# Kernel tuning notes

Measured on AMD Instinct MI355X. Metric: run time of the kernel, lower is better.

Reference implementation:

```python
import jax, jax.numpy as jnp
import numpy as np

# dims
N, D, H, C = 50000, 64, 4, 64          # nodes, node feat (=out_channels), heads, head dim
E, P, EPN, V, NA = 300000, 20000, 300000, 2000, 128  # node edges, paths, path->node edges, vehicles, n_actor
HC = H * C
HID = (NA + D) // 2                    # PathPredNet hidden (size // 2)


def _layernorm(x, g, b, eps=1e-5):
    m = x.mean(-1, keepdims=True)
    v = ((x - m) ** 2).mean(-1, keepdims=True)
    return (x - m) * jax.lax.rsqrt(v + eps) * g + b


def _segment_softmax(logits, seg, num):
    m = jax.ops.segment_max(logits, seg, num_segments=num)
    e = jnp.exp(logits - m[seg])
    s = jax.ops.segment_sum(e, seg, num_segments=num)
    return e / (s[seg] + 1e-16)


def setup_inputs() -> dict:
    key = jax.random.key(0)
    ks = jax.random.split(key, 32)

    def lin(k, i, o):
        s = 1.0 / np.sqrt(i)
        return jax.random.uniform(k, (i, o), minval=-s, maxval=s, dtype=jnp.float32)

    inp = {}
    inp['x'] = jax.random.normal(ks[0], (N, D), dtype=jnp.float32)
    inp['edge_index'] = jax.random.randint(ks[1], (2, E), 0, N)
    inp['path_node_u'] = jax.random.randint(ks[2], (EPN,), 0, P)
    inp['path_node_v'] = jax.random.randint(ks[3], (EPN,), 0, N)
    inp['veh_path_u'] = jax.random.randint(ks[4], (P,), 0, V)
    inp['actors'] = jax.random.normal(ks[5], (V, NA), dtype=jnp.float32)
    # TransformerConv params
    inp['Wq'] = lin(ks[6], D, HC);  inp['bq'] = jnp.zeros((HC,), jnp.float32)
    inp['Wk'] = lin(ks[7], D, HC);  inp['bk'] = jnp.zeros((HC,), jnp.float32)
    inp['Wv'] = lin(ks[8], D, HC);  inp['bv'] = jnp.zeros((HC,), jnp.float32)
    inp['Wskip'] = lin(ks[9], HC, D); inp['bskip'] = jnp.zeros((D,), jnp.float32)
    inp['ln1_g'] = jnp.ones((D,), jnp.float32); inp['ln1_b'] = jnp.zeros((D,), jnp.float32)
    inp['Wf1'] = lin(ks[10], D, 2 * D); inp['bf1'] = jnp.zeros((2 * D,), jnp.float32)
    inp['Wf2'] = lin(ks[11], 2 * D, D); inp['bf2'] = jnp.zeros((D,), jnp.float32)
    inp['ln2_g'] = jnp.ones((D,), jnp.float32); inp['ln2_b'] = jnp.zeros((D,), jnp.float32)
    # PathPredNet params (non-latent: size = n_actor + n_map)
    inp['Wp1'] = lin(ks[12], NA + D, HID); inp['bp1'] = jnp.zeros((HID,), jnp.float32)
    inp['gn_g'] = jnp.ones((HID,), jnp.float32); inp['gn_b'] = jnp.zeros((HID,), jnp.float32)
    inp['Wp2'] = lin(ks[13], HID, 1); inp['bp2'] = jnp.zeros((1,), jnp.float32)
    return inp


def reference(x, edge_index, path_node_u, path_node_v, veh_path_u, actors,
              Wq, bq, Wk, bk, Wv, bv, Wskip, bskip, ln1_g, ln1_b,
              Wf1, bf1, Wf2, bf2, ln2_g, ln2_b,
              Wp1, bp1, gn_g, gn_b, Wp2, bp2):
    # ---- TransformerConv (multi-head graph attention over edge list) ----
    q = (x @ Wq + bq).reshape(N, H, C)
    k = (x @ Wk + bk).reshape(N, H, C)
    v = (x @ Wv + bv).reshape(N, H, C)
    src, dst = edge_index[0], edge_index[1]
    alpha = (q[dst] * k[src]).sum(-1) / np.sqrt(C)           # [E, H]
    a = _segment_softmax(alpha, dst, N)                      # edge softmax per target node
    msg = v[src] * a[:, :, None]                             # [E, H, C]
    out = jax.ops.segment_sum(msg, dst, num_segments=N).reshape(N, HC)
    out = out @ Wskip + bskip                                # lin_skip (concat path)
    out = _layernorm(out + x, ln1_g, ln1_b)                  # norm1(out + x)
    ff = jax.nn.relu(out @ Wf1 + bf1) @ Wf2 + bf2            # feed_forward
    out2 = _layernorm(ff + x, ln2_g, ln2_b)                  # norm2(ff + x) -- residual is x as in source

    # ---- path features: aggregate member-node features per path (path->node edges) ----
    psum = jax.ops.segment_sum(out2[path_node_v], path_node_u, num_segments=P)
    cnt = jax.ops.segment_sum(jnp.ones((EPN,), out2.dtype), path_node_u, num_segments=P)
    paths = psum / jnp.maximum(cnt, 1.0)[:, None]            # [P, D]

    # ---- PathPredNet: logit per (veh, path) edge; veh_path_u[p] is owner vehicle ----
    feat = jnp.concatenate([paths, actors[veh_path_u]], axis=-1)  # [P, D + NA]
    h = feat @ Wp1 + bp1
    hm = h.mean(-1, keepdims=True)
    hv = ((h - hm) ** 2).mean(-1, keepdims=True)
    h = jax.nn.relu((h - hm) * jax.lax.rsqrt(hv + 1e-5) * gn_g + gn_b)   # GN with ng=1
    logits = (h @ Wp2 + bp2).squeeze(-1)                     # [P]

    # ---- scatter_softmax over each vehicle's candidate paths (ucb_sample_path) ----
    probs = _segment_softmax(logits, veh_path_u, V)          # [P]
    return (out2, probs)
```

## Files before the change

### kernel.cpp

```cpp
#include <hip/hip_runtime.h>
#include <hip/hip_bf16.h>
#include <math.h>

#define N_    50000
#define D_    64
#define H_    4
#define C_    64
#define HC_   256
#define E_    300000
#define P_    20000
#define EPN_  300000
#define V_    2000
#define NA_   128
#define HID_  96

#define CN_        70000
#define SCAN_CHUNK 4096
#define SCAN_NB    18

typedef __attribute__((ext_vector_type(8))) short bf16x8;
typedef __attribute__((ext_vector_type(4))) float f32x4;

__device__ __forceinline__ unsigned short f2bf(float f) {
    unsigned u = __float_as_uint(f);
    unsigned r = (u + 0x7fffu + ((u >> 16) & 1u)) >> 16;
    return (unsigned short)r;
}
__device__ __forceinline__ float bf2f(unsigned short u) {
    return __uint_as_float(((unsigned)u) << 16);
}

__device__ __forceinline__ void atomicMaxFloat(float* addr, float value) {
    if (value >= 0.f)
        atomicMax((int*)addr, __float_as_int(value));
    else
        atomicMin((unsigned int*)addr, __float_as_uint(value));
}

__device__ __forceinline__ float waveRedSum(float v) {
    #pragma unroll
    for (int off = 32; off; off >>= 1) v += __shfl_xor(v, off);
    return v;
}
__device__ __forceinline__ int waveRedSumI(int v) {
    #pragma unroll
    for (int off = 32; off; off >>= 1) v += __shfl_xor(v, off);
    return v;
}

__global__ void neginf_kernel(float* __restrict__ p, int n) {
    int i = blockIdx.x * 256 + threadIdx.x;
    if (i < n) p[i] = __int_as_float(0xFF800000);
}

__global__ void hist_kernel(const int* __restrict__ ei, const int* __restrict__ pnu,
                            int* __restrict__ deg_n, int* __restrict__ deg_p) {
    int i = blockIdx.x * 256 + threadIdx.x;
    if (i < E_) {
        atomicAdd(&deg_n[ei[E_ + i]], 1);
    } else if (i < E_ + EPN_) {
        atomicAdd(&deg_p[pnu[i - E_]], 1);
    }
}

__global__ __launch_bounds__(256) void scan_part_kernel(
    const int* __restrict__ cdeg, int* __restrict__ bsum) {
    __shared__ int wred[4];
    int b = blockIdx.x, t = threadIdx.x;
    int base = b * SCAN_CHUNK + t * 16;
    int s = 0;
    #pragma unroll
    for (int j = 0; j < 16; j += 4) {
        int idx = base + j;
        if (idx + 3 < CN_) {
            int4 vv = *(const int4*)(cdeg + idx);
            s += vv.x + vv.y + vv.z + vv.w;
        } else {
            #pragma unroll
            for (int q = 0; q < 4; ++q) if (idx + q < CN_) s += cdeg[idx + q];
        }
    }
    s = waveRedSumI(s);
    if ((t & 63) == 0) wred[t >> 6] = s;
    __syncthreads();
    if (t == 0) bsum[b] = wred[0] + wred[1] + wred[2] + wred[3];
}

__global__ void scan_bsum_kernel(int* __restrict__ bsum) {
    int t = threadIdx.x;
    int o = (t < SCAN_NB) ? bsum[t] : 0;
    int v = o;
    #pragma unroll
    for (int d = 1; d < 64; d <<= 1) {
        int x = __shfl_up(v, d);
        if (t >= d) v += x;
    }
    if (t < SCAN_NB) bsum[t] = v - o;
}

__global__ __launch_bounds__(256) void scan_write_kernel(
    const int* __restrict__ cdeg, const int* __restrict__ bof,
    int* __restrict__ start_n, int* __restrict__ start_p) {
    __shared__ int th[256];
    int b = blockIdx.x, t = threadIdx.x;
    int base = b * SCAN_CHUNK + t * 16;
    int v[16];
    int s = 0;
    #pragma unroll
    for (int j = 0; j < 16; j += 4) {
        int idx = base + j;
        if (idx + 3 < CN_) {
            int4 vv = *(const int4*)(cdeg + idx);
            v[j] = vv.x; v[j + 1] = vv.y; v[j + 2] = vv.z; v[j + 3] = vv.w;
        } else {
            #pragma unroll
            for (int q = 0; q < 4; ++q) v[j + q] = (idx + q < CN_) ? cdeg[idx + q] : 0;
        }
        s += v[j] + v[j + 1] + v[j + 2] + v[j + 3];
    }
    th[t] = s;
    __syncthreads();
    for (int d = 1; d < 256; d <<= 1) {
        int x = (t >= d) ? th[t - d] : 0;
        __syncthreads();
        th[t] += x;
        __syncthreads();
    }
    int off = bof[b] + th[t] - s;
    #pragma unroll
    for (int j = 0; j < 16; ++j) {
        int idx = base + j;
        if (idx < CN_) {
            if (idx < N_) start_n[idx] = off;
            else          start_p[idx - N_] = off - E_;
            off += v[j];
        }
    }
    if (b == 0 && t == 0) { start_n[N_] = E_; start_p[P_] = EPN_; }
}

__global__ void fill_kernel(const int* __restrict__ ei, const int* __restrict__ pnu,
                            const int* __restrict__ pnv,
                            const int* __restrict__ start_n, const int* __restrict__ start_p,
                            int* __restrict__ cur_n, int* __restrict__ cur_p,
                            int* __restrict__ csr_n, int* __restrict__ csr_p) {
    int i = blockIdx.x * 256 + threadIdx.x;
    if (i < E_) {
        int dst = ei[E_ + i];
        int pos = atomicAdd(&cur_n[dst], 1);
        csr_n[start_n[dst] + pos] = ei[i];
    } else if (i < E_ + EPN_) {
        int j = i - E_;
        int u = pnu[j];
        int pos = atomicAdd(&cur_p[u], 1);
        csr_p[start_p[u] + pos] = pnv[j];
    }
}

__global__ __launch_bounds__(256) void prep_pack_kernel(
    const float* __restrict__ Wq, const float* __restrict__ Wk, const float* __restrict__ Wv,
    const float* __restrict__ Wskip, const float* __restrict__ Wf1, const float* __restrict__ Wf2,
    const float* __restrict__ Wp1, unsigned short* __restrict__ frags) {
    int tid = blockIdx.x * 256 + threadIdx.x;
    int f = tid >> 6, l = tid & 63;
    if (f >= 196) return;
    const float* W; int ld, nt, kb;
    if (f < 96)       { int mat = f >> 5, r = f & 31; nt = r >> 1; kb = r & 1;
                        W = (mat == 0) ? Wq : (mat == 1) ? Wk : Wv; ld = 256; }
    else if (f < 128) { int g = f - 96;  nt = g >> 3; kb = g & 7; W = Wskip; ld = 64; }
    else if (f < 144) { int g = f - 128; nt = g >> 1; kb = g & 1; W = Wf1;   ld = 128; }
    else if (f < 160) { int g = f - 144; nt = g >> 2; kb = g & 3; W = Wf2;   ld = 64; }
    else              { int g = f - 160; nt = g / 6;  kb = g % 6; W = Wp1;   ld = 96; }
    int k0 = kb * 32 + (l >> 4) * 8;
    int c  = nt * 16 + (l & 15);
    unsigned short o[8];
    #pragma unroll
    for (int j = 0; j < 8; ++j) o[j] = f2bf(W[(k0 + j) * ld + c]);
    unsigned short* dst = frags + (size_t)f * 512 + l * 8;
    ((uint4*)dst)[0] = *(const uint4*)o;
}

__global__ __launch_bounds__(256) void proj_mfma_kernel(
    const float* __restrict__ x, const unsigned short* __restrict__ frags,
    const float* __restrict__ bq, const float* __restrict__ bk, const float* __restrict__ bv,
    unsigned short* __restrict__ qb, unsigned short* __restrict__ kbuf,
    unsigned short* __restrict__ vbuf) {
    int w = threadIdx.x >> 6, l = threadIdx.x & 63;
    int rbase = blockIdx.x * 64 + w * 16;
    int rA = rbase + (l & 15);
    int lg = l >> 4;
    bf16x8 a[2];
    #pragma unroll
    for (int kb = 0; kb < 2; ++kb) {
        int k0 = kb * 32 + lg * 8;
        float4 p0 = {0, 0, 0, 0}, p1 = {0, 0, 0, 0};
        if (rA < N_) {
            p0 = *(const float4*)(x + (size_t)rA * 64 + k0);
            p1 = *(const float4*)(x + (size_t)rA * 64 + k0 + 4);
        }
        a[kb][0] = (short)f2bf(p0.x); a[kb][1] = (short)f2bf(p0.y);
        a[kb][2] = (short)f2bf(p0.z); a[kb][3] = (short)f2bf(p0.w);
        a[kb][4] = (short)f2bf(p1.x); a[kb][5] = (short)f2bf(p1.y);
        a[kb][6] = (short)f2bf(p1.z); a[kb][7] = (short)f2bf(p1.w);
    }
    int row0 = rbase + lg * 4;
    int cl = l & 15;
    for (int nt = 0; nt < 48; ++nt) {
        int mat = nt >> 4, ntl = nt & 15;
        const unsigned short* fp = frags + (size_t)(nt * 2) * 512 + l * 8;
        bf16x8 b0 = *(const bf16x8*)fp;
        bf16x8 b1 = *(const bf16x8*)(fp + 512);
        f32x4 acc = {0.f, 0.f, 0.f, 0.f};
        acc = __builtin_amdgcn_mfma_f32_16x16x32_bf16(a[0], b0, acc, 0, 0, 0);
        acc = __builtin_amdgcn_mfma_f32_16x16x32_bf16(a[1], b1, acc, 0, 0, 0);
        int col = ntl * 16 + cl;
        const float* bias = (mat == 0) ? bq : (mat == 1) ? bk : bv;
        unsigned short* out = (mat == 0) ? qb : (mat == 1) ? kbuf : vbuf;
        float bsv = bias[col];
        #pragma unroll
        for (int r = 0; r < 4; ++r) {
            int row = row0 + r;
            if (row < N_) out[(size_t)row * 256 + col] = f2bf(acc[r] + bsv);
        }
    }
}

__global__ __launch_bounds__(256) void attn_gather_kernel(
    const int* __restrict__ start, const int* __restrict__ csr,
    const unsigned short* __restrict__ qb, const unsigned short* __restrict__ kbuf,
    const unsigned short* __restrict__ vbuf, float* __restrict__ agg) {
    int n = blockIdx.x * 4 + (threadIdx.x >> 6);
    if (n >= N_) return;
    int l = threadIdx.x & 63;
    ushort4 q4 = ((const ushort4*)(qb + (size_t)n * 256))[l];
    float qx = bf2f(q4.x), qy = bf2f(q4.y), qz = bf2f(q4.z), qw = bf2f(q4.w);
    int s0 = start[n], s1 = start[n + 1];
    float m = -INFINITY, ssum = 0.f;
    float ax = 0.f, ay = 0.f, az = 0.f, aw = 0.f;
    for (int i = s0; i < s1; ++i) {
        int src = csr[i];
        ushort4 k4 = ((const ushort4*)(kbuf + (size_t)src * 256))[l];
        ushort4 v4 = ((const ushort4*)(vbuf + (size_t)src * 256))[l];
        float p = qx * bf2f(k4.x) + qy * bf2f(k4.y) + qz * bf2f(k4.z) + qw * bf2f(k4.w);
        p += __shfl_xor(p, 1); p += __shfl_xor(p, 2);
        p += __shfl_xor(p, 4); p += __shfl_xor(p, 8);
        p *= 0.125f;
        float mn = fmaxf(m, p);
        float sc = expf(m - mn);
        float wt = expf(p - mn);
        ssum = ssum * sc + wt;
        ax = ax * sc + bf2f(v4.x) * wt;
        ay = ay * sc + bf2f(v4.y) * wt;
        az = az * sc + bf2f(v4.z) * wt;
        aw = aw * sc + bf2f(v4.w) * wt;
        m = mn;
    }
    float inv = 1.f / (ssum + 1e-16f);
    float4 o;
    o.x = ax * inv; o.y = ay * inv; o.z = az * inv; o.w = aw * inv;
    ((float4*)(agg + (size_t)n * 256))[l] = o;
}

__global__ __launch_bounds__(256) void post_mfma_kernel(
    const float* __restrict__ agg, const float* __restrict__ x,
    const unsigned short* __restrict__ frags,
    const float* __restrict__ bskip,
    const float* __restrict__ ln1g, const float* __restrict__ ln1b,
    const float* __restrict__ bf1v, const float* __restrict__ bf2v,
    const float* __restrict__ ln2g, const float* __restrict__ ln2b,
    float* __restrict__ out2) {
    __shared__ float h1s[32][64];
    __shared__ unsigned short ls[32 * 64];
    __shared__ unsigned short f1s[32 * 128];
    int w = threadIdx.x >> 6, l = threadIdx.x & 63;
    int rblk = blockIdx.x * 32;
    int mt = w >> 1;
    int ntbase = (w & 1) * 2;
    int lr = l & 15, lg = l >> 4;

    {
        f32x4 acc0 = {0.f, 0.f, 0.f, 0.f}, acc1 = {0.f, 0.f, 0.f, 0.f};
        int rA = rblk + mt * 16 + lr;
        for (int kb = 0; kb < 8; ++kb) {
            int k0 = kb * 32 + lg * 8;
            bf16x8 a;
            float4 p0 = {0, 0, 0, 0}, p1 = {0, 0, 0, 0};
            if (rA < N_) {
                p0 = *(const float4*)(agg + (size_t)rA * 256 + k0);
                p1 = *(const float4*)(agg + (size_t)rA * 256 + k0 + 4);
            }
            a[0] = (short)f2bf(p0.x); a[1] = (short)f2bf(p0.y);
            a[2] = (short)f2bf(p0.z); a[3] = (short)f2bf(p0.w);
            a[4] = (short)f2bf(p1.x); a[5] = (short)f2bf(p1.y);
            a[6] = (short)f2bf(p1.z); a[7] = (short)f2bf(p1.w);
            bf16x8 b0 = *(const bf16x8*)(frags + (size_t)(96 + (ntbase + 0) * 8 + kb) * 512 + l * 8);
            bf16x8 b1 = *(const bf16x8*)(frags + (size_t)(96 + (ntbase + 1) * 8 + kb) * 512 + l * 8);
            acc0 = __builtin_amdgcn_mfma_f32_16x16x32_bf16(a, b0, acc0, 0, 0, 0);
            acc1 = __builtin_amdgcn_mfma_f32_16x16x32_bf16(a, b1, acc1, 0, 0, 0);
        }
        int lrow0 = mt * 16 + lg * 4;
        #pragma unroll
        for (int t2 = 0; t2 < 2; ++t2) {
            f32x4 acc = t2 ? acc1 : acc0;
            int col = (ntbase + t2) * 16 + lr;
            float bsv = bskip[col];
            #pragma unroll
            for (int r = 0; r < 4; ++r) {
                int grow = rblk + lrow0 + r;
                float xv = (grow < N_) ? x[(size_t)grow * 64 + col] : 0.f;
                h1s[lrow0 + r][col] = acc[r] + bsv + xv;
            }
        }
    }
    __syncthreads();
    #pragma unroll
    for (int i = 0; i < 8; ++i) {
        int r = w * 8 + i;
        float vv = h1s[r][l];
        float mean = waveRedSum(vv) * (1.f / 64.f);
        float d = vv - mean;
        float var = waveRedSum(d * d) * (1.f / 64.f);
        float l1 = d * rsqrtf(var + 1e-5f) * ln1g[l] + ln1b[l];
        int byte = r * 128 + ((l * 2) ^ ((r & 7) << 4));
        ls[byte >> 1] = f2bf(l1);
    }
    __syncthreads();
    {
        int rB = mt * 16 + lr;
        bf16x8 a0, a1;
        {
            int b0off = rB * 128 + (((0 * 32 + lg * 8) * 2) ^ ((rB & 7) << 4));
            int b1off = rB * 128 + (((1 * 32 + lg * 8) * 2) ^ ((rB & 7) << 4));
            a0 = *(const bf16x8*)((const char*)ls + b0off);
            a1 = *(const bf16x8*)((const char*)ls + b1off);
        }
        #pragma unroll
        for (int j = 0; j < 4; ++j) {
            int nt = (w & 1) * 4 + j;
            bf16x8 b0 = *(const bf16x8*)(frags + (size_t)(128 + nt * 2 + 0) * 512 + l * 8);
            bf16x8 b1 = *(const bf16x8*)(frags + (size_t)(128 + nt * 2 + 1) * 512 + l * 8);
            f32x4 acc = {0.f, 0.f, 0.f, 0.f};
            acc = __builtin_amdgcn_mfma_f32_16x16x32_bf16(a0, b0, acc, 0, 0, 0);
            acc = __builtin_amdgcn_mfma_f32_16x16x32_bf16(a1, b1, acc, 0, 0, 0);
            int col = nt * 16 + lr;
            float bb = bf1v[col];
            #pragma unroll
            for (int r = 0; r < 4; ++r) {
                int lrow = mt * 16 + lg * 4 + r;
                float fv = fmaxf(acc[r] + bb, 0.f);
                int byte = lrow * 256 + ((col * 2) ^ ((lrow & 7) << 4));
                f1s[byte >> 1] = f2bf(fv);
            }
        }
    }
    __syncthreads();
    {
        int rC = mt * 16 + lr;
        bf16x8 a[4];
        #pragma unroll
        for (int kb = 0; kb < 4; ++kb) {
            int k0 = kb * 32 + lg * 8;
            int byte = rC * 256 + ((k0 * 2) ^ ((rC & 7) << 4));
            a[kb] = *(const bf16x8*)((const char*)f1s + byte);
        }
        int lrow0 = mt * 16 + lg * 4;
        f32x4 accs[2];
        #pragma unroll
        for (int t2 = 0; t2 < 2; ++t2) {
            int nt = ntbase + t2;
            f32x4 acc = {0.f, 0.f, 0.f, 0.f};
            #pragma unroll
            for (int kb = 0; kb < 4; ++kb) {
                bf16x8 b = *(const bf16x8*)(frags + (size_t)(144 + nt * 4 + kb) * 512 + l * 8);
                acc = __builtin_amdgcn_mfma_f32_16x16x32_bf16(a[kb], b, acc, 0, 0, 0);
            }
            accs[t2] = acc;
        }
        __syncthreads();
        #pragma unroll
        for (int t2 = 0; t2 < 2; ++t2) {
            int col = (ntbase + t2) * 16 + lr;
            float bb = bf2v[col];
            #pragma unroll
            for (int r = 0; r < 4; ++r) {
                int grow = rblk + lrow0 + r;
                float xv = (grow < N_) ? x[(size_t)grow * 64 + col] : 0.f;
                h1s[lrow0 + r][col] = accs[t2][r] + bb + xv;
            }
        }
    }
    __syncthreads();
    #pragma unroll
    for (int i = 0; i < 8; ++i) {
        int r = w * 8 + i;
        int grow = rblk + r;
        float vv = h1s[r][l];
        float mean = waveRedSum(vv) * (1.f / 64.f);
        float d = vv - mean;
        float var = waveRedSum(d * d) * (1.f / 64.f);
        float o = d * rsqrtf(var + 1e-5f) * ln2g[l] + ln2b[l];
        if (grow < N_) out2[(size_t)grow * 64 + l] = o;
    }
}

__global__ __launch_bounds__(256) void path_gather_kernel(
    const int* __restrict__ start, const int* __restrict__ csr,
    const float* __restrict__ out2, float* __restrict__ pmean) {
    int p = blockIdx.x * 4 + (threadIdx.x >> 6);
    if (p >= P_) return;
    int lane = threadIdx.x & 63;
    int s0 = start[p], s1 = start[p + 1];
    float sum = 0.f;
    for (int i = s0; i < s1; ++i)
        sum += out2[(size_t)csr[i] * 64 + lane];
    pmean[(size_t)p * 64 + lane] = sum / fmaxf((float)(s1 - s0), 1.f);
}

__global__ __launch_bounds__(256) void pred_mfma_kernel(
    const float* __restrict__ pmean, const int* __restrict__ vehu,
    const float* __restrict__ actors, const unsigned short* __restrict__ frags,
    const float* __restrict__ bp1, const float* __restrict__ gng,
    const float* __restrict__ gnb, const float* __restrict__ Wp2,
    const float* __restrict__ bp2, float* __restrict__ logits, float* __restrict__ vm) {
    int w = threadIdx.x >> 6, l = threadIdx.x & 63;
    int p0 = blockIdx.x * 64 + w * 16;
    if (p0 >= P_) return;
    int lr = l & 15, lg = l >> 4;
    int pA = p0 + lr;
    bool valid = pA < P_;
    int veh = valid ? vehu[pA] : 0;
    bf16x8 a[6];
    #pragma unroll
    for (int kb = 0; kb < 6; ++kb) {
        int k0 = kb * 32 + lg * 8;
        float4 q0 = {0, 0, 0, 0}, q1 = {0, 0, 0, 0};
        if (valid) {
            if (k0 < 64) {
                q0 = *(const float4*)(pmean + (size_t)pA * 64 + k0);
                q1 = *(const float4*)(pmean + (size_t)pA * 64 + k0 + 4);
            } else {
                q0 = *(const float4*)(actors + (size_t)veh * 128 + (k0 - 64));
                q1 = *(const float4*)(actors + (size_t)veh * 128 + (k0 - 64) + 4);
            }
        }
        a[kb][0] = (short)f2bf(q0.x); a[kb][1] = (short)f2bf(q0.y);
        a[kb][2] = (short)f2bf(q0.z); a[kb][3] = (short)f2bf(q0.w);
        a[kb][4] = (short)f2bf(q1.x); a[kb][5] = (short)f2bf(q1.y);
        a[kb][6] = (short)f2bf(q1.z); a[kb][7] = (short)f2bf(q1.w);
    }
    f32x4 acc[6];
    #pragma unroll
    for (int nt = 0; nt < 6; ++nt) acc[nt] = (f32x4){0.f, 0.f, 0.f, 0.f};
    #pragma unroll
    for (int kb = 0; kb < 6; ++kb) {
        #pragma unroll
        for (int nt = 0; nt < 6; ++nt) {
            bf16x8 b = *(const bf16x8*)(frags + (size_t)(160 + nt * 6 + kb) * 512 + l * 8);
            acc[nt] = __builtin_amdgcn_mfma_f32_16x16x32_bf16(a[kb], b, acc[nt], 0, 0, 0);
        }
    }
    float gg[6], gb[6], w2v[6];
    #pragma unroll
    for (int nt = 0; nt < 6; ++nt) {
        int col = nt * 16 + lr;
        float bb = bp1[col];
        #pragma unroll
        for (int r = 0; r < 4; ++r) acc[nt][r] += bb;
        gg[nt] = gng[col]; gb[nt] = gnb[col]; w2v[nt] = Wp2[col];
    }
    float b2 = bp2[0];
    #pragma unroll
    for (int r = 0; r < 4; ++r) {
        float s = 0.f;
        #pragma unroll
        for (int nt = 0; nt < 6; ++nt) s += acc[nt][r];
        s += __shfl_xor(s, 1); s += __shfl_xor(s, 2);
        s += __shfl_xor(s, 4); s += __shfl_xor(s, 8);
        float mean = s * (1.f / 96.f);
        float qv = 0.f;
        #pragma unroll
        for (int nt = 0; nt < 6; ++nt) { float d = acc[nt][r] - mean; qv += d * d; }
        qv += __shfl_xor(qv, 1); qv += __shfl_xor(qv, 2);
        qv += __shfl_xor(qv, 4); qv += __shfl_xor(qv, 8);
        float rstd = rsqrtf(qv * (1.f / 96.f) + 1e-5f);
        float t = 0.f;
        #pragma unroll
        for (int nt = 0; nt < 6; ++nt) {
            float d = (acc[nt][r] - mean) * rstd * gg[nt] + gb[nt];
            t += fmaxf(d, 0.f) * w2v[nt];
        }
        t += __shfl_xor(t, 1); t += __shfl_xor(t, 2);
        t += __shfl_xor(t, 4); t += __shfl_xor(t, 8);
        int prow = p0 + lg * 4 + r;
        if (lr == 0 && prow < P_) {
            float logit = t + b2;
            logits[prow] = logit;
            atomicMaxFloat(&vm[vehu[prow]], logit);
        }
    }
}

__global__ void vexp_kernel(float* __restrict__ logits, const float* __restrict__ vm,
                            const int* __restrict__ vehu, float* __restrict__ vs) {
    int p = blockIdx.x * 256 + threadIdx.x;
    if (p >= P_) return;
    int veh = vehu[p];
    float e = expf(logits[p] - vm[veh]);
    logits[p] = e;
    unsafeAtomicAdd(&vs[veh], e);
}

__global__ void prob_kernel(const float* __restrict__ logits, const float* __restrict__ vs,
                            const int* __restrict__ vehu, float* __restrict__ probs) {
    int p = blockIdx.x * 256 + threadIdx.x;
    if (p >= P_) return;
    probs[p] = logits[p] / (vs[vehu[p]] + 1e-16f);
}

extern "C" void kernel_launch(void* const* d_in, const int* in_sizes, int n_in,
                              void* d_out, int out_size, void* d_ws, size_t ws_size,
                              hipStream_t stream) {
    const float* x      = (const float*)d_in[0];
    const int*   ei     = (const int*)d_in[1];
    const int*   pnu    = (const int*)d_in[2];
    const int*   pnv    = (const int*)d_in[3];
    const int*   vpu    = (const int*)d_in[4];
    const float* actors = (const float*)d_in[5];
    const float* Wq = (const float*)d_in[6];  const float* bq = (const float*)d_in[7];
    const float* Wk = (const float*)d_in[8];  const float* bk = (const float*)d_in[9];
    const float* Wv = (const float*)d_in[10]; const float* bv = (const float*)d_in[11];
    const float* Wskip = (const float*)d_in[12]; const float* bskip = (const float*)d_in[13];
    const float* ln1g = (const float*)d_in[14]; const float* ln1b = (const float*)d_in[15];
    const float* Wf1 = (const float*)d_in[16]; const float* bf1 = (const float*)d_in[17];
    const float* Wf2 = (const float*)d_in[18]; const float* bf2 = (const float*)d_in[19];
    const float* ln2g = (const float*)d_in[20]; const float* ln2b = (const float*)d_in[21];
    const float* Wp1 = (const float*)d_in[22]; const float* bp1 = (const float*)d_in[23];
    const float* gng = (const float*)d_in[24]; const float* gnb = (const float*)d_in[25];
    const float* Wp2 = (const float*)d_in[26]; const float* bp2 = (const float*)d_in[27];

    float* ws = (float*)d_ws;
    unsigned short* qb    = (unsigned short*)(ws);
    unsigned short* kbuf  = (unsigned short*)(ws + 6400000);
    unsigned short* vbuf  = (unsigned short*)(ws + 12800000);
    float* agg    = ws + 19200000;
    unsigned short* frags = (unsigned short*)(ws + 32000000);
    int*   deg_n  = (int*)(ws + 32050200);
    int*   deg_p  = (int*)(ws + 32100200);
    float* vs     = ws + 32120200;
    int*   start_n= (int*)(ws + 32122200);
    int*   start_p= (int*)(ws + 32172201);
    int*   csr_n  = (int*)(ws + 32192202);
    int*   csr_p  = (int*)(ws + 32492202);
    float* pmean  = ws + 32792202;
    float* logits = ws + 34072202;
    float* vm     = ws + 34092202;
    int*   bsum   = (int*)(ws + 34094202);

    float* out2  = (float*)d_out;
    float* probs = out2 + (size_t)N_ * 64;

    hipMemsetAsync(deg_n, 0, 72000 * sizeof(int), stream);
    neginf_kernel<<<(V_ + 255) / 256, 256, 0, stream>>>(vm, V_);

    prep_pack_kernel<<<49, 256, 0, stream>>>(Wq, Wk, Wv, Wskip, Wf1, Wf2, Wp1, frags);
    int histGrid = (E_ + EPN_ + 255) / 256;
    hist_kernel<<<histGrid, 256, 0, stream>>>(ei, pnu, deg_n, deg_p);
    scan_part_kernel<<<SCAN_NB, 256, 0, stream>>>(deg_n, bsum);
    scan_bsum_kernel<<<1, 64, 0, stream>>>(bsum);
    scan_write_kernel<<<SCAN_NB, 256, 0, stream>>>(deg_n, bsum, start_n, start_p);
    hipMemsetAsync(deg_n, 0, 70000 * sizeof(int), stream);
    fill_kernel<<<histGrid, 256, 0, stream>>>(ei, pnu, pnv, start_n, start_p,
                                              deg_n, deg_p, csr_n, csr_p);

    proj_mfma_kernel<<<(N_ + 63) / 64, 256, 0, stream>>>(x, frags, bq, bk, bv, qb, kbuf, vbuf);
    attn_gather_kernel<<<(N_ + 3) / 4, 256, 0, stream>>>(start_n, csr_n, qb, kbuf, vbuf, agg);
    post_mfma_kernel<<<(N_ + 31) / 32, 256, 0, stream>>>(agg, x, frags, bskip, ln1g, ln1b,
                                                         bf1, bf2, ln2g, ln2b, out2);
    path_gather_kernel<<<P_ / 4, 256, 0, stream>>>(start_p, csr_p, out2, pmean);
    pred_mfma_kernel<<<(P_ + 63) / 64, 256, 0, stream>>>(pmean, vpu, actors, frags, bp1,
                                                         gng, gnb, Wp2, bp2, logits, vm);
    vexp_kernel<<<(P_ + 255) / 256, 256, 0, stream>>>(logits, vm, vpu, vs);
    prob_kernel<<<(P_ + 255) / 256, 256, 0, stream>>>(logits, vs, vpu, probs);
}
```

Baseline: 381.0 us.

## Unroll attention gather by two edges, use exp2, store aggregate as bf16 in place

```diff
diff --git a/kernel.cpp b/kernel.cpp
--- a/kernel.cpp
+++ b/kernel.cpp
@@ -227,42 +227,87 @@
 
 __global__ __launch_bounds__(256) void attn_gather_kernel(
     const int* __restrict__ start, const int* __restrict__ csr,
-    const unsigned short* __restrict__ qb, const unsigned short* __restrict__ kbuf,
-    const unsigned short* __restrict__ vbuf, float* __restrict__ agg) {
+    unsigned short* __restrict__ qb, const unsigned short* __restrict__ kbuf,
+    const unsigned short* __restrict__ vbuf) {
     int n = blockIdx.x * 4 + (threadIdx.x >> 6);
     if (n >= N_) return;
     int l = threadIdx.x & 63;
     ushort4 q4 = ((const ushort4*)(qb + (size_t)n * 256))[l];
     float qx = bf2f(q4.x), qy = bf2f(q4.y), qz = bf2f(q4.z), qw = bf2f(q4.w);
-    int s0 = start[n], s1 = start[n + 1];
-    float m = -INFINITY, ssum = 0.f;
-    float ax = 0.f, ay = 0.f, az = 0.f, aw = 0.f;
-    for (int i = s0; i < s1; ++i) {
-        int src = csr[i];
-        ushort4 k4 = ((const ushort4*)(kbuf + (size_t)src * 256))[l];
-        ushort4 v4 = ((const ushort4*)(vbuf + (size_t)src * 256))[l];
-        float p = qx * bf2f(k4.x) + qy * bf2f(k4.y) + qz * bf2f(k4.z) + qw * bf2f(k4.w);
-        p += __shfl_xor(p, 1); p += __shfl_xor(p, 2);
-        p += __shfl_xor(p, 4); p += __shfl_xor(p, 8);
-        p *= 0.125f;
-        float mn = fmaxf(m, p);
-        float sc = expf(m - mn);
-        float wt = expf(p - mn);
-        ssum = ssum * sc + wt;
-        ax = ax * sc + bf2f(v4.x) * wt;
-        ay = ay * sc + bf2f(v4.y) * wt;
-        az = az * sc + bf2f(v4.z) * wt;
-        aw = aw * sc + bf2f(v4.w) * wt;
-        m = mn;
-    }
-    float inv = 1.f / (ssum + 1e-16f);
-    float4 o;
-    o.x = ax * inv; o.y = ay * inv; o.z = az * inv; o.w = aw * inv;
-    ((float4*)(agg + (size_t)n * 256))[l] = o;
+    int e0 = start[n], e1 = start[n + 1];
+    const float SCL = 0.18033688f;
+    float m0 = -INFINITY, s0 = 0.f, a0x = 0.f, a0y = 0.f, a0z = 0.f, a0w = 0.f;
+    float m1 = -INFINITY, s1 = 0.f, a1x = 0.f, a1y = 0.f, a1z = 0.f, a1w = 0.f;
+    int i = e0;
+    for (; i + 1 < e1; i += 2) {
+        int srcA = csr[i], srcB = csr[i + 1];
+        ushort4 kA = ((const ushort4*)(kbuf + (size_t)srcA * 256))[l];
+        ushort4 vA = ((const ushort4*)(vbuf + (size_t)srcA * 256))[l];
+        ushort4 kB = ((const ushort4*)(kbuf + (size_t)srcB * 256))[l];
+        ushort4 vB = ((const ushort4*)(vbuf + (size_t)srcB * 256))[l];
+        float pA = qx * bf2f(kA.x) + qy * bf2f(kA.y) + qz * bf2f(kA.z) + qw * bf2f(kA.w);
+        float pB = qx * bf2f(kB.x) + qy * bf2f(kB.y) + qz * bf2f(kB.z) + qw * bf2f(kB.w);
+        pA += __shfl_xor(pA, 1); pB += __shfl_xor(pB, 1);
+        pA += __shfl_xor(pA, 2); pB += __shfl_xor(pB, 2);
+        pA += __shfl_xor(pA, 4); pB += __shfl_xor(pB, 4);
+        pA += __shfl_xor(pA, 8); pB += __shfl_xor(pB, 8);
+        pA *= SCL; pB *= SCL;
+        float mn0 = fmaxf(m0, pA);
+        float c0 = exp2f(m0 - mn0);
+        float w0 = exp2f(pA - mn0);
+        s0 = s0 * c0 + w0;
+        a0x = a0x * c0 + bf2f(vA.x) * w0;
+        a0y = a0y * c0 + bf2f(vA.y) * w0;
+        a0z = a0z * c0 + bf2f(vA.z) * w0;
+        a0w = a0w * c0 + bf2f(vA.w) * w0;
+        m0 = mn0;
+        float mn1 = fmaxf(m1, pB);
+        float c1 = exp2f(m1 - mn1);
+        float w1 = exp2f(pB - mn1);
+        s1 = s1 * c1 + w1;
+        a1x = a1x * c1 + bf2f(vB.x) * w1;
+        a1y = a1y * c1 + bf2f(vB.y) * w1;
+        a1z = a1z * c1 + bf2f(vB.z) * w1;
+        a1w = a1w * c1 + bf2f(vB.w) * w1;
+        m1 = mn1;
+    }
+    if (i < e1) {
+        int srcA = csr[i];
+        ushort4 kA = ((const ushort4*)(kbuf + (size_t)srcA * 256))[l];
+        ushort4 vA = ((const ushort4*)(vbuf + (size_t)srcA * 256))[l];
+        float pA = qx * bf2f(kA.x) + qy * bf2f(kA.y) + qz * bf2f(kA.z) + qw * bf2f(kA.w);
+        pA += __shfl_xor(pA, 1); pA += __shfl_xor(pA, 2);
+        pA += __shfl_xor(pA, 4); pA += __shfl_xor(pA, 8);
+        pA *= SCL;
+        float mn0 = fmaxf(m0, pA);
+        float c0 = exp2f(m0 - mn0);
+        float w0 = exp2f(pA - mn0);
+        s0 = s0 * c0 + w0;
+        a0x = a0x * c0 + bf2f(vA.x) * w0;
+        a0y = a0y * c0 + bf2f(vA.y) * w0;
+        a0z = a0z * c0 + bf2f(vA.z) * w0;
+        a0w = a0w * c0 + bf2f(vA.w) * w0;
+        m0 = mn0;
+    }
+    float o0 = 0.f, o1 = 0.f, o2 = 0.f, o3 = 0.f;
+    float mm = fmaxf(m0, m1);
+    if (mm > -INFINITY) {
+        float c0 = exp2f(m0 - mm);
+        float c1 = exp2f(m1 - mm);
+        float ss = s0 * c0 + s1 * c1;
+        float inv = 1.f / (ss + 1e-16f);
+        o0 = (a0x * c0 + a1x * c1) * inv;
+        o1 = (a0y * c0 + a1y * c1) * inv;
+        o2 = (a0z * c0 + a1z * c1) * inv;
+        o3 = (a0w * c0 + a1w * c1) * inv;
+    }
+    ushort4 o;
+    o.x = f2bf(o0); o.y = f2bf(o1); o.z = f2bf(o2); o.w = f2bf(o3);
+    ((ushort4*)(qb + (size_t)n * 256))[l] = o;
 }
 
 __global__ __launch_bounds__(256) void post_mfma_kernel(
-    const float* __restrict__ agg, const float* __restrict__ x,
+    const unsigned short* __restrict__ aggb, const float* __restrict__ x,
     const unsigned short* __restrict__ frags,
     const float* __restrict__ bskip,
     const float* __restrict__ ln1g, const float* __restrict__ ln1b,
@@ -283,16 +328,8 @@
         int rA = rblk + mt * 16 + lr;
         for (int kb = 0; kb < 8; ++kb) {
             int k0 = kb * 32 + lg * 8;
-            bf16x8 a;
-            float4 p0 = {0, 0, 0, 0}, p1 = {0, 0, 0, 0};
-            if (rA < N_) {
-                p0 = *(const float4*)(agg + (size_t)rA * 256 + k0);
-                p1 = *(const float4*)(agg + (size_t)rA * 256 + k0 + 4);
-            }
-            a[0] = (short)f2bf(p0.x); a[1] = (short)f2bf(p0.y);
-            a[2] = (short)f2bf(p0.z); a[3] = (short)f2bf(p0.w);
-            a[4] = (short)f2bf(p1.x); a[5] = (short)f2bf(p1.y);
-            a[6] = (short)f2bf(p1.z); a[7] = (short)f2bf(p1.w);
+            bf16x8 a = {0, 0, 0, 0, 0, 0, 0, 0};
+            if (rA < N_) a = *(const bf16x8*)(aggb + (size_t)rA * 256 + k0);
             bf16x8 b0 = *(const bf16x8*)(frags + (size_t)(96 + (ntbase + 0) * 8 + kb) * 512 + l * 8);
             bf16x8 b1 = *(const bf16x8*)(frags + (size_t)(96 + (ntbase + 1) * 8 + kb) * 512 + l * 8);
             acc0 = __builtin_amdgcn_mfma_f32_16x16x32_bf16(a, b0, acc0, 0, 0, 0);
@@ -542,7 +579,6 @@
     unsigned short* qb    = (unsigned short*)(ws);
     unsigned short* kbuf  = (unsigned short*)(ws + 6400000);
     unsigned short* vbuf  = (unsigned short*)(ws + 12800000);
-    float* agg    = ws + 19200000;
     unsigned short* frags = (unsigned short*)(ws + 32000000);
     int*   deg_n  = (int*)(ws + 32050200);
     int*   deg_p  = (int*)(ws + 32100200);
@@ -573,8 +609,8 @@
                                               deg_n, deg_p, csr_n, csr_p);
 
     proj_mfma_kernel<<<(N_ + 63) / 64, 256, 0, stream>>>(x, frags, bq, bk, bv, qb, kbuf, vbuf);
-    attn_gather_kernel<<<(N_ + 3) / 4, 256, 0, stream>>>(start_n, csr_n, qb, kbuf, vbuf, agg);
-    post_mfma_kernel<<<(N_ + 31) / 32, 256, 0, stream>>>(agg, x, frags, bskip, ln1g, ln1b,
+    attn_gather_kernel<<<(N_ + 3) / 4, 256, 0, stream>>>(start_n, csr_n, qb, kbuf, vbuf);
+    post_mfma_kernel<<<(N_ + 31) / 32, 256, 0, stream>>>(qb, x, frags, bskip, ln1g, ln1b,
                                                          bf1, bf2, ln2g, ln2b, out2);
     path_gather_kernel<<<P_ / 4, 256, 0, stream>>>(start_p, csr_p, out2, pmean);
     pred_mfma_kernel<<<(P_ + 63) / 64, 256, 0, stream>>>(pmean, vpu, actors, frags, bp1,
```

Result: faster. 366.4 us (-3.8%).
